# Performance work log

Hardware: AMD Instinct MI355X
Metric: run time of the kernel (lower is better)

The kernel has to match this reference:

```python
import jax, jax.numpy as jnp
import numpy as np

NUM_HEADS = 14
SCALE = 0.125  # fixed constant in the source, not 1/sqrt(head_dim)
PATCH = 14
DIM = 3 * PATCH * PATCH  # 588


def setup_inputs() -> dict:
    key = jax.random.key(0)
    k_x, k_cw, k_cb, k_qw, k_qb = jax.random.split(key, 5)
    B, C_in, H, W = 8, 3, 448, 448
    x = jax.random.normal(k_x, (B, C_in, H, W), dtype=jnp.float32)
    # Conv2d(in_channels=3, dim, kernel=patch, stride=patch), torch layout OIHW
    fan_in = C_in * PATCH * PATCH
    bound = 1.0 / np.sqrt(fan_in)
    conv_w = jax.random.uniform(k_cw, (DIM, C_in, PATCH, PATCH), jnp.float32, -bound, bound)
    conv_b = jax.random.uniform(k_cb, (DIM,), jnp.float32, -bound, bound)
    # Linear(dim, 3*dim): weight [out, in] torch layout
    lb = 1.0 / np.sqrt(DIM)
    qkv_w = jax.random.uniform(k_qw, (3 * DIM, DIM), jnp.float32, -lb, lb)
    qkv_b = jax.random.uniform(k_qb, (3 * DIM,), jnp.float32, -lb, lb)
    return {"x": x, "conv_w": conv_w, "conv_b": conv_b, "qkv_w": qkv_w, "qkv_b": qkv_b}


def reference(x, conv_w, conv_b, qkv_w, qkv_b):
    # Patch embedding: conv kernel==stride==patch  -> [B, DIM, H/p, W/p]
    y = jax.lax.conv_general_dilated(
        x, conv_w, window_strides=(PATCH, PATCH), padding="VALID",
        dimension_numbers=("NCHW", "OIHW", "NCHW"))
    y = y + conv_b[None, :, None, None]
    B = y.shape[0]
    # flatten(2).transpose(1, 2) -> [B, N, C]
    tokens = y.reshape(B, DIM, -1).transpose(0, 2, 1)
    N, C = tokens.shape[1], tokens.shape[2]
    hd = C // NUM_HEADS  # 42
    qkv = tokens @ qkv_w.T + qkv_b  # [B, N, 3C]
    qkv = qkv.reshape(B, N, 3, NUM_HEADS, hd).transpose(2, 0, 3, 1, 4)  # [3,B,H,N,hd]
    q, k, v = qkv[0], qkv[1], qkv[2]
    attn = jnp.einsum("bhnd,bhmd->bhnm", q, k) * SCALE  # [B,H,N,N]
    attn = jax.nn.softmax(attn, axis=-1)
    out = jnp.einsum("bhnm,bhmd->bhnd", attn, v)  # [B,H,N,hd]
    out = out.transpose(0, 2, 1, 3).reshape(B, N, C)  # [B,N,C]
    return out
```

## Files before the change

### kernel.cpp

```cpp
#include <hip/hip_runtime.h>

typedef unsigned short u16;
typedef unsigned int u32;
typedef unsigned long long u64;
typedef __attribute__((ext_vector_type(8))) short bf16x8;
typedef __attribute__((ext_vector_type(4))) float f32x4;

#define MTOK 8192
#define KP   640
#define CC   588
#define C3   1764
#define NH   14
#define SEQ  1024
#define HD   42
#define DP   64
#define DV   48
#define SC2f 0.18033688011112042f

static __device__ __forceinline__ u16 f2b(float f) {
  unsigned u = __builtin_bit_cast(unsigned, f);
  u = (u + 0x7FFFu + ((u >> 16) & 1u)) >> 16;
  return (u16)u;
}

static __device__ __forceinline__ void gl_lds16(const void* g, void* l) {
  auto gp = (const unsigned int __attribute__((address_space(1)))*)((unsigned long long)g);
  auto lp = (unsigned int __attribute__((address_space(3)))*)((unsigned long long)l);
  __builtin_amdgcn_global_load_lds(gp, lp, 16, 0, 0);
}

static __device__ __forceinline__ u32 pk2(float lo, float hi) {
  u32 a = __builtin_bit_cast(u32, lo) + 0x8000u;
  u32 b = __builtin_bit_cast(u32, hi) + 0x8000u;
  return __builtin_amdgcn_perm(b, a, 0x07060302u);
}

__global__ void im2col_k(const float* __restrict__ x, u16* __restrict__ A,
                         u16* __restrict__ vT, u16* __restrict__ qb, u16* __restrict__ kb) {
  int t = blockIdx.x;
  int b = t >> 10, pi = t & 1023, ph = pi >> 5, pw = pi & 31;
  const float* xb = x + (size_t)b * 3 * 448 * 448;
  u32* Arow = (u32*)(A + (size_t)t * KP);
  for (int h = threadIdx.x; h < KP / 2; h += 256) {
    int kk = h * 2;
    u32 v = 0;
    if (kk < CC) {
      int c = kk / 196, rem = kk - c * 196, i = rem / 14, j = rem - i * 14;
      const float* p = &xb[(size_t)(c * 448 + ph * 14 + i) * 448 + pw * 14 + j];
      v = pk2(p[0], p[1]);
    }
    Arow[h] = v;
  }
  if (t < 112) {
    u16* row = vT + ((size_t)(t * DV + HD)) * SEQ;
    for (int n = threadIdx.x; n < SEQ; n += 256) row[n] = 0x3F80;
    for (int n = threadIdx.x; n < SEQ; n += 256) {
      u64* pq = (u64*)&qb[((size_t)t * SEQ + n) * DP + 40];
      u64* pk = (u64*)&kb[((size_t)t * SEQ + n) * DP + 40];
#pragma unroll
      for (int z = 0; z < 3; z++) { pq[z] = 0; pk[z] = 0; }
    }
  }
}

__global__ void padw_k(const float* __restrict__ wc, const float* __restrict__ wq,
                       u16* __restrict__ dc, u16* __restrict__ dq) {
  int r = blockIdx.x;
  const float* src; u16* dst; int R, rr;
  if (r < 640) { src = wc; dst = dc; R = CC; rr = r; }
  else         { src = wq; dst = dq; R = C3; rr = r - 640; }
  for (int c = threadIdx.x; c < KP; c += 256) {
    float v = (rr < R && c < CC) ? src[(size_t)rr * CC + c] : 0.f;
    dst[(size_t)rr * KP + c] = f2b(v);
  }
}

template <int MODE>
__global__ void __launch_bounds__(256, 2) gemm_k(
    const u16* __restrict__ A, const u16* __restrict__ Bt,
    const float* __restrict__ bias, u16* __restrict__ out0,
    u16* __restrict__ qb, u16* __restrict__ kb, u16* __restrict__ vb) {
  __shared__ alignas(16) u16 sA[128 * 64];
  __shared__ alignas(16) u16 sB[128 * 64];
  const int tid = threadIdx.x;
  const int wave = tid >> 6, lane = tid & 63, quad = lane >> 4, l16 = lane & 15;
  const int wi = wave >> 1, wj = wave & 1;
  const int m0 = blockIdx.x * 128, n0 = blockIdx.y * 128;
  const int rL = lane >> 3, scid = lane & 7;
  const f32x4 z4 = {0.f, 0.f, 0.f, 0.f};

  f32x4 acc[4][4];
#pragma unroll
  for (int i = 0; i < 4; i++)
#pragma unroll
    for (int j = 0; j < 4; j++) acc[i][j] = z4;

  for (int k0 = 0; k0 < KP; k0 += 64) {
    __syncthreads();
#pragma unroll
    for (int cc = wave; cc < 16; cc += 4) {
      int r = cc * 8 + rL;
      gl_lds16(A + ((size_t)(m0 + r) * KP + k0 + (scid ^ (r & 7)) * 8), &sA[cc * 512]);
    }
#pragma unroll
    for (int cc = wave; cc < 16; cc += 4) {
      int r = cc * 8 + rL;
      gl_lds16(Bt + ((size_t)(n0 + r) * KP + k0 + (scid ^ (r & 7)) * 8), &sB[cc * 512]);
    }
    __syncthreads();
#pragma unroll
    for (int ks = 0; ks < 2; ks++) {
      bf16x8 af[4], bfr[4];
#pragma unroll
      for (int i = 0; i < 4; i++) {
        int r = wi * 64 + i * 16 + l16;
        af[i] = *(const bf16x8*)&sA[r * 64 + (((ks * 4 + quad) ^ (r & 7)) * 8)];
      }
#pragma unroll
      for (int j = 0; j < 4; j++) {
        int r = wj * 64 + j * 16 + l16;
        bfr[j] = *(const bf16x8*)&sB[r * 64 + (((ks * 4 + quad) ^ (r & 7)) * 8)];
      }
#pragma unroll
      for (int i = 0; i < 4; i++)
#pragma unroll
        for (int j = 0; j < 4; j++)
          acc[i][j] = __builtin_amdgcn_mfma_f32_16x16x32_bf16(af[i], bfr[j], acc[i][j], 0, 0, 0);
    }
  }

  const int baser = wi * 64 + quad * 4;
  if (MODE == 0) {
#pragma unroll
    for (int j = 0; j < 4; j++) {
      int col = n0 + wj * 64 + j * 16 + l16;
      float bs = (col < CC) ? bias[col] : 0.f;
#pragma unroll
      for (int i = 0; i < 4; i++) {
        int row = m0 + baser + i * 16;
#pragma unroll
        for (int r = 0; r < 4; r++)
          out0[(size_t)(row + r) * KP + col] = f2b(acc[i][j][r] + bs);
      }
    }
  } else {
#pragma unroll
    for (int j = 0; j < 4; j++) {
      int col = n0 + wj * 64 + j * 16 + l16;
      if (col < C3) {
        float bs = bias[col];
        int which = col / CC;
        int rem = col - which * CC;
        int h = rem / HD;
        int d = rem - h * HD;
        if (which < 2) {
          u16* dst = (which == 0) ? qb : kb;
          float sc = (which == 0) ? SC2f : 1.0f;
#pragma unroll
          for (int i = 0; i < 4; i++) {
            int row = m0 + baser + i * 16;
#pragma unroll
            for (int r = 0; r < 4; r++) {
              int rw = row + r;
              int b = rw >> 10, n = rw & 1023;
              dst[((size_t)((b * NH + h) * SEQ + n)) * DP + d] = f2b((acc[i][j][r] + bs) * sc);
            }
          }
        } else {
#pragma unroll
          for (int i = 0; i < 4; i++) {
            int row = m0 + baser + i * 16;
            int b = row >> 10, n = row & 1023;
            u64 pk = (u64)f2b(acc[i][j][0] + bs) | ((u64)f2b(acc[i][j][1] + bs) << 16) |
                     ((u64)f2b(acc[i][j][2] + bs) << 32) | ((u64)f2b(acc[i][j][3] + bs) << 48);
            *(u64*)&vb[((size_t)((b * NH + h) * DV + d)) * SEQ + n] = pk;
          }
        }
      }
    }
  }
}

__global__ void __launch_bounds__(256) attn_k(
    const u16* __restrict__ qb, const u16* __restrict__ kb,
    const u16* __restrict__ vT, float* __restrict__ out) {
  __shared__ alignas(16) u16 sK[64 * 64];
  __shared__ alignas(16) u16 sV[DV * 64];
  __shared__ alignas(16) u16 sP[4][32 * 72];
  const int tid = threadIdx.x;
  const int wave = tid >> 6, lane = tid & 63, quad = lane >> 4, l16 = lane & 15;
  const int g = blockIdx.x;
  const int bh = (g & 7) * 14 + (g >> 6);
  const int qt = (g >> 3) & 7;
  const int q0 = qt * 128;
  const int rL = lane >> 3, scid = lane & 7;
  const f32x4 z4 = {0.f, 0.f, 0.f, 0.f};
  u16* sPw = sP[wave];

  bf16x8 aq[2][2];
#pragma unroll
  for (int i = 0; i < 2; i++) {
    const u16* qrow = qb + ((size_t)(bh * SEQ + q0 + wave * 32 + i * 16 + l16)) * DP;
    aq[i][0] = *(const bf16x8*)&qrow[quad * 8];
    aq[i][1] = *(const bf16x8*)&qrow[32 + quad * 8];
  }
  f32x4 o[2][3];
#pragma unroll
  for (int i = 0; i < 2; i++)
#pragma unroll
    for (int j = 0; j < 3; j++) o[i][j] = z4;

  const u16* kb0 = kb + (size_t)bh * SEQ * DP;
  const u16* vb0 = vT + (size_t)bh * DV * SEQ;

  for (int kt = 0; kt < 16; kt++) {
    const int m0 = kt * 64;
    __syncthreads();
#pragma unroll
    for (int cc = wave; cc < 8; cc += 4) {
      int r = cc * 8 + rL;
      gl_lds16(kb0 + ((size_t)(m0 + r)) * DP + (scid ^ ((r >> 2) & 7)) * 8, &sK[cc * 512]);
    }
#pragma unroll
    for (int cc = wave; cc < 6; cc += 4) {
      int d = cc * 8 + rL;
      gl_lds16(vb0 + (size_t)d * SEQ + m0 + (scid ^ (d & 7)) * 8, &sV[cc * 512]);
    }
    __syncthreads();
    bf16x8 bk[4][2];
#pragma unroll
    for (int j = 0; j < 4; j++) {
      int rr = 4 * l16 + j;
#pragma unroll
      for (int ks = 0; ks < 2; ks++)
        bk[j][ks] = *(const bf16x8*)&sK[rr * 64 + (((ks * 4 + quad) ^ (l16 & 7)) * 8)];
    }
#pragma unroll
    for (int i = 0; i < 2; i++) {
      f32x4 s[4];
#pragma unroll
      for (int j = 0; j < 4; j++) {
        f32x4 t = __builtin_amdgcn_mfma_f32_16x16x32_bf16(aq[i][0], bk[j][0], z4, 0, 0, 0);
        s[j] = __builtin_amdgcn_mfma_f32_16x16x32_bf16(aq[i][1], bk[j][1], t, 0, 0, 0);
      }
#pragma unroll
      for (int r = 0; r < 4; r++) {
        u32 d0 = pk2(__builtin_amdgcn_exp2f(s[0][r]), __builtin_amdgcn_exp2f(s[1][r]));
        u32 d1 = pk2(__builtin_amdgcn_exp2f(s[2][r]), __builtin_amdgcn_exp2f(s[3][r]));
        u32* dst = (u32*)&sPw[(i * 16 + quad * 4 + r) * 72 + l16 * 4];
        dst[0] = d0;
        dst[1] = d1;
      }
    }
#pragma unroll
    for (int ks = 0; ks < 2; ks++) {
      bf16x8 bv[3];
#pragma unroll
      for (int j = 0; j < 3; j++) {
        int d = j * 16 + l16;
        bv[j] = *(const bf16x8*)&sV[d * 64 + (((ks * 4 + quad) ^ (d & 7)) * 8)];
      }
#pragma unroll
      for (int i = 0; i < 2; i++) {
        bf16x8 ap = *(const bf16x8*)&sPw[(i * 16 + l16) * 72 + ks * 32 + quad * 8];
#pragma unroll
        for (int j = 0; j < 3; j++)
          o[i][j] = __builtin_amdgcn_mfma_f32_16x16x32_bf16(ap, bv[j], o[i][j], 0, 0, 0);
      }
    }
  }

  const int b = bh / NH, h = bh - b * NH;
#pragma unroll
  for (int i = 0; i < 2; i++) {
#pragma unroll
    for (int r = 0; r < 4; r++) {
      float ls = __shfl(o[i][2][r], (lane & 48) + 10, 64);
      float rc = 1.f / ls;
      int row = wave * 32 + i * 16 + quad * 4 + r;
      float* orow = out + ((size_t)(b * SEQ + q0 + row)) * CC + h * HD;
#pragma unroll
      for (int j = 0; j < 3; j++) {
        int d = j * 16 + l16;
        if (d < HD) orow[d] = o[i][j][r] * rc;
      }
    }
  }
}

extern "C" void kernel_launch(void* const* d_in, const int* in_sizes, int n_in,
                              void* d_out, int out_size, void* d_ws, size_t ws_size,
                              hipStream_t stream) {
  (void)in_sizes; (void)n_in; (void)out_size; (void)ws_size;
  const float* x      = (const float*)d_in[0];
  const float* conv_w = (const float*)d_in[1];
  const float* conv_b = (const float*)d_in[2];
  const float* qkv_w  = (const float*)d_in[3];
  const float* qkv_b  = (const float*)d_in[4];
  float* out = (float*)d_out;

  char* ws = (char*)d_ws;
  size_t off = 0;
  u16* A      = (u16*)(ws + off); off += (size_t)MTOK * KP * 2;
  u16* Wc     = (u16*)(ws + off); off += (size_t)640 * KP * 2;
  u16* Wq     = (u16*)(ws + off); off += (size_t)1792 * KP * 2;
  u16* tokens = (u16*)(ws + off); off += (size_t)MTOK * KP * 2;
  u16* qbuf   = (u16*)(ws + off); off += (size_t)112 * SEQ * DP * 2;
  u16* kbuf   = (u16*)(ws + off); off += (size_t)112 * SEQ * DP * 2;
  u16* vTb    = (u16*)(ws + off); off += (size_t)112 * DV * SEQ * 2;

  im2col_k<<<MTOK, 256, 0, stream>>>(x, A, vTb, qbuf, kbuf);
  padw_k<<<2432, 256, 0, stream>>>(conv_w, qkv_w, Wc, Wq);
  gemm_k<0><<<dim3(64, 5), 256, 0, stream>>>(A, Wc, conv_b, tokens, nullptr, nullptr, nullptr);
  gemm_k<1><<<dim3(64, 14), 256, 0, stream>>>(tokens, Wq, qkv_b, nullptr, qbuf, kbuf, vTb);
  attn_k<<<896, 256, 0, stream>>>(qbuf, kbuf, vTb, out);
}
```

Baseline: 182.6 us.

## Merge prep kernels and stage Q/K epilogue through LDS for coalesced stores

```diff
diff --git a/kernel.cpp b/kernel.cpp
--- a/kernel.cpp
+++ b/kernel.cpp
@@ -35,43 +35,44 @@
   return __builtin_amdgcn_perm(b, a, 0x07060302u);
 }
 
-__global__ void im2col_k(const float* __restrict__ x, u16* __restrict__ A,
-                         u16* __restrict__ vT, u16* __restrict__ qb, u16* __restrict__ kb) {
+__global__ void prep_k(const float* __restrict__ x, u16* __restrict__ A,
+                       u16* __restrict__ vT, u16* __restrict__ qb, u16* __restrict__ kb,
+                       const float* __restrict__ wc, const float* __restrict__ wq,
+                       u16* __restrict__ Wc, u16* __restrict__ Wq) {
   int t = blockIdx.x;
-  int b = t >> 10, pi = t & 1023, ph = pi >> 5, pw = pi & 31;
-  const float* xb = x + (size_t)b * 3 * 448 * 448;
-  u32* Arow = (u32*)(A + (size_t)t * KP);
-  for (int h = threadIdx.x; h < KP / 2; h += 256) {
-    int kk = h * 2;
-    u32 v = 0;
-    if (kk < CC) {
-      int c = kk / 196, rem = kk - c * 196, i = rem / 14, j = rem - i * 14;
-      const float* p = &xb[(size_t)(c * 448 + ph * 14 + i) * 448 + pw * 14 + j];
-      v = pk2(p[0], p[1]);
-    }
-    Arow[h] = v;
-  }
-  if (t < 112) {
-    u16* row = vT + ((size_t)(t * DV + HD)) * SEQ;
-    for (int n = threadIdx.x; n < SEQ; n += 256) row[n] = 0x3F80;
-    for (int n = threadIdx.x; n < SEQ; n += 256) {
-      u64* pq = (u64*)&qb[((size_t)t * SEQ + n) * DP + 40];
-      u64* pk = (u64*)&kb[((size_t)t * SEQ + n) * DP + 40];
-#pragma unroll
-      for (int z = 0; z < 3; z++) { pq[z] = 0; pk[z] = 0; }
-    }
-  }
-}
-
-__global__ void padw_k(const float* __restrict__ wc, const float* __restrict__ wq,
-                       u16* __restrict__ dc, u16* __restrict__ dq) {
-  int r = blockIdx.x;
-  const float* src; u16* dst; int R, rr;
-  if (r < 640) { src = wc; dst = dc; R = CC; rr = r; }
-  else         { src = wq; dst = dq; R = C3; rr = r - 640; }
-  for (int c = threadIdx.x; c < KP; c += 256) {
-    float v = (rr < R && c < CC) ? src[(size_t)rr * CC + c] : 0.f;
-    dst[(size_t)rr * KP + c] = f2b(v);
+  if (t < MTOK) {
+    int b = t >> 10, pi = t & 1023, ph = pi >> 5, pw = pi & 31;
+    const float* xb = x + (size_t)b * 3 * 448 * 448;
+    u32* Arow = (u32*)(A + (size_t)t * KP);
+    for (int h = threadIdx.x; h < KP / 2; h += 256) {
+      int kk = h * 2;
+      u32 v = 0;
+      if (kk < CC) {
+        int c = kk / 196, rem = kk - c * 196, i = rem / 14, j = rem - i * 14;
+        const float* p = &xb[(size_t)(c * 448 + ph * 14 + i) * 448 + pw * 14 + j];
+        v = pk2(p[0], p[1]);
+      }
+      Arow[h] = v;
+    }
+    if (t < 112) {
+      u16* row = vT + ((size_t)(t * DV + HD)) * SEQ;
+      for (int n = threadIdx.x; n < SEQ; n += 256) row[n] = 0x3F80;
+      for (int n = threadIdx.x; n < SEQ; n += 256) {
+        u64* pq = (u64*)&qb[((size_t)t * SEQ + n) * DP + 40];
+        u64* pk = (u64*)&kb[((size_t)t * SEQ + n) * DP + 40];
+#pragma unroll
+        for (int z = 0; z < 3; z++) { pq[z] = 0; pk[z] = 0; }
+      }
+    }
+  } else {
+    int r = t - MTOK;
+    const float* src; u16* dst; int R, rr;
+    if (r < 640) { src = wc; dst = Wc; R = CC; rr = r; }
+    else         { src = wq; dst = Wq; R = C3; rr = r - 640; }
+    for (int c = threadIdx.x; c < KP; c += 256) {
+      float v = (rr < R && c < CC) ? src[(size_t)rr * CC + c] : 0.f;
+      dst[(size_t)rr * KP + c] = f2b(v);
+    }
   }
 }
 
@@ -80,8 +81,9 @@
     const u16* __restrict__ A, const u16* __restrict__ Bt,
     const float* __restrict__ bias, u16* __restrict__ out0,
     u16* __restrict__ qb, u16* __restrict__ kb, u16* __restrict__ vb) {
-  __shared__ alignas(16) u16 sA[128 * 64];
-  __shared__ alignas(16) u16 sB[128 * 64];
+  __shared__ alignas(16) u16 smem[128 * 136];
+  u16* sA = smem;
+  u16* sB = smem + 128 * 64;
   const int tid = threadIdx.x;
   const int wave = tid >> 6, lane = tid & 63, quad = lane >> 4, l16 = lane & 15;
   const int wi = wave >> 1, wj = wave & 1;
@@ -144,29 +146,16 @@
       }
     }
   } else {
+    __syncthreads();
 #pragma unroll
     for (int j = 0; j < 4; j++) {
       int col = n0 + wj * 64 + j * 16 + l16;
       if (col < C3) {
         float bs = bias[col];
         int which = col / CC;
-        int rem = col - which * CC;
-        int h = rem / HD;
-        int d = rem - h * HD;
-        if (which < 2) {
-          u16* dst = (which == 0) ? qb : kb;
-          float sc = (which == 0) ? SC2f : 1.0f;
-#pragma unroll
-          for (int i = 0; i < 4; i++) {
-            int row = m0 + baser + i * 16;
-#pragma unroll
-            for (int r = 0; r < 4; r++) {
-              int rw = row + r;
-              int b = rw >> 10, n = rw & 1023;
-              dst[((size_t)((b * NH + h) * SEQ + n)) * DP + d] = f2b((acc[i][j][r] + bs) * sc);
-            }
-          }
-        } else {
+        if (which == 2) {
+          int rem = col - 2 * CC;
+          int h = rem / HD, d = rem - h * HD;
 #pragma unroll
           for (int i = 0; i < 4; i++) {
             int row = m0 + baser + i * 16;
@@ -174,6 +163,37 @@
             u64 pk = (u64)f2b(acc[i][j][0] + bs) | ((u64)f2b(acc[i][j][1] + bs) << 16) |
                      ((u64)f2b(acc[i][j][2] + bs) << 32) | ((u64)f2b(acc[i][j][3] + bs) << 48);
             *(u64*)&vb[((size_t)((b * NH + h) * DV + d)) * SEQ + n] = pk;
+          }
+        } else {
+          float sc = (which == 0) ? SC2f : 1.0f;
+          int lcol = wj * 64 + j * 16 + l16;
+#pragma unroll
+          for (int i = 0; i < 4; i++) {
+            int lrow = baser + i * 16;
+#pragma unroll
+            for (int r = 0; r < 4; r++)
+              smem[(lrow + r) * 136 + lcol] = f2b((acc[i][j][r] + bs) * sc);
+          }
+        }
+      }
+    }
+    __syncthreads();
+    {
+      const int c2 = 2 * (tid & 63);
+      const int w = tid >> 6;
+      int gcol = n0 + c2;
+      if (gcol < C3) {
+        int which = gcol / CC;
+        if (which < 2) {
+          int rem = gcol - which * CC;
+          int h = rem / HD, d = rem - h * HD;
+          u16* dstp = (which == 0) ? qb : kb;
+          const int b = m0 >> 10, nb = m0 & 1023;
+          u32* base = (u32*)&dstp[((size_t)((b * NH + h) * SEQ + nb)) * DP + d];
+#pragma unroll
+          for (int rr = 0; rr < 32; rr++) {
+            int row = w * 32 + rr;
+            base[(size_t)row * (DP / 2)] = *(const u32*)&smem[row * 136 + c2];
           }
         }
       }
@@ -309,8 +329,7 @@
   u16* kbuf   = (u16*)(ws + off); off += (size_t)112 * SEQ * DP * 2;
   u16* vTb    = (u16*)(ws + off); off += (size_t)112 * DV * SEQ * 2;
 
-  im2col_k<<<MTOK, 256, 0, stream>>>(x, A, vTb, qbuf, kbuf);
-  padw_k<<<2432, 256, 0, stream>>>(conv_w, qkv_w, Wc, Wq);
+  prep_k<<<MTOK + 2432, 256, 0, stream>>>(x, A, vTb, qbuf, kbuf, conv_w, qkv_w, Wc, Wq);
   gemm_k<0><<<dim3(64, 5), 256, 0, stream>>>(A, Wc, conv_b, tokens, nullptr, nullptr, nullptr);
   gemm_k<1><<<dim3(64, 14), 256, 0, stream>>>(tokens, Wq, qkv_b, nullptr, qbuf, kbuf, vTb);
   attn_k<<<896, 256, 0, stream>>>(qbuf, kbuf, vTb, out);
```

After: 173.7 us. 4.8% less time.
